# Kernel tuning notes

Measured on AMD Instinct MI355X. Metric: run time of the kernel, lower is better.

The kernel has to match this reference:

```python
import jax, jax.numpy as jnp
import numpy as np

DIM = 512

def setup_inputs() -> dict:
    key = jax.random.key(0)
    ks = jax.random.split(key, 7)
    B, Nq, Nkv = 8, 1024, 4096
    prototype = jax.random.normal(ks[0], (B, Nq, DIM), dtype=jnp.float32)
    q_x = jax.random.normal(ks[1], (B, Nkv, DIM), dtype=jnp.float32)
    qry_attn_mask = jax.random.bernoulli(ks[2], 0.5, (B, Nkv))  # True = keep
    # Linear(dim, dim, bias=False) weights, torch convention y = x @ W.T
    s = 1.0 / np.sqrt(DIM)
    Wq = jax.random.uniform(ks[3], (DIM, DIM), jnp.float32, -s, s)
    Wk = jax.random.uniform(ks[4], (DIM, DIM), jnp.float32, -s, s)
    Wv = jax.random.uniform(ks[5], (DIM, DIM), jnp.float32, -s, s)
    Wproj = jax.random.uniform(ks[6], (DIM, DIM), jnp.float32, -s, s)
    return {"prototype": prototype, "q_x": q_x, "qry_attn_mask": qry_attn_mask,
            "Wq": Wq, "Wk": Wk, "Wv": Wv, "Wproj": Wproj}

def reference(prototype, q_x, qry_attn_mask, Wq, Wk, Wv, Wproj):
    scale = DIM ** (-0.5)
    q = jnp.einsum('bnd,ed->bne', prototype, Wq)          # [B,Nq,D]
    k = jnp.einsum('bmd,ed->bme', q_x, Wk)                # [B,Nkv,D]
    v = jnp.einsum('bmd,ed->bme', q_x, Wv)                # [B,Nkv,D]
    attn = jnp.einsum('bnd,bmd->bnm', q, k) * scale       # [B,Nq,Nkv]
    bias = (~qry_attn_mask).astype(attn.dtype)[:, None, :] * -10000.0
    attn = jax.nn.softmax(attn + bias, axis=-1)
    x = jnp.einsum('bnm,bmd->bnd', attn, v)
    x = jnp.einsum('bnd,ed->bne', x, Wproj)
    return x
```

## Files before the change

### kernel.cpp

```cpp
#include <hip/hip_runtime.h>
#include <hip/hip_bf16.h>
#include <stdint.h>


typedef __bf16 bf16;
typedef bf16 bf16x8 __attribute__((ext_vector_type(8)));
typedef bf16 bf16x4 __attribute__((ext_vector_type(4)));
typedef float f32x4 __attribute__((ext_vector_type(4)));

#define NB 8
#define NQ 1024
#define NKV 4096
#define DD 512
#define RT_LD 136

__device__ __forceinline__ void lds16(const bf16* g, bf16* l) {
  __builtin_amdgcn_global_load_lds(
      (const __attribute__((address_space(1))) unsigned int*)g,
      (__attribute__((address_space(3))) unsigned int*)l, 16, 0, 0);
}

__global__ void scan_mask(const void* __restrict__ mask,
                          int* __restrict__ idx, int* __restrict__ cnt,
                          int* __restrict__ kpad, float* __restrict__ denom) {
  const int b = blockIdx.x, tid = threadIdx.x;
  for (int i = tid; i < NQ; i += 256) denom[b * NQ + i] = 0.f;

  __shared__ int s0, s1;
  if (tid == 0) { s0 = 0; s1 = 0; }
  __syncthreads();
  {
    const unsigned* mw = (const unsigned*)mask;
    int b0 = 0, b1 = 0;
    for (int i = tid; i < 8192; i += 256) {
      unsigned v = mw[i];
      if (v > 1u) b0 = 1;
      if (v != 0u && v != 0x3F800000u) b1 = 1;
    }
    if (b0) atomicOr(&s0, 1);
    if (b1) atomicOr(&s1, 1);
  }
  __syncthreads();
  const int mode = (s0 == 0) ? 0 : ((s1 == 0) ? 1 : 2);

  __shared__ int ps[256];
  unsigned bits = 0;
  int c = 0;
  const int base = tid * 16;
  for (int i = 0; i < 16; ++i) {
    const int col = base + i;
    bool k;
    if (mode == 0)      k = ((const int*)mask)[b * NKV + col] != 0;
    else if (mode == 1) k = ((const float*)mask)[b * NKV + col] != 0.f;
    else                k = ((const unsigned char*)mask)[b * NKV + col] != 0;
    bits |= (unsigned)k << i;
    c += k;
  }
  ps[tid] = c;
  __syncthreads();
  for (int s = 1; s < 256; s <<= 1) {
    int v = (tid >= s) ? ps[tid - s] : 0;
    __syncthreads();
    ps[tid] += v;
    __syncthreads();
  }
  int off = ps[tid] - c;
  for (int i = 0; i < 16; ++i)
    if ((bits >> i) & 1) idx[b * NKV + off++] = base + i;
  if (tid == 255) {
    cnt[b] = ps[255];
    kpad[b] = (ps[255] + 127) & ~127;
  }
}

__global__ void prep(const float* __restrict__ qx, const int* __restrict__ idx,
                     const int* __restrict__ cnt, const int* __restrict__ kpad,
                     bf16* __restrict__ qc,
                     const float* __restrict__ proto, bf16* __restrict__ proto_b,
                     const float* __restrict__ Wq, const float* __restrict__ Wk,
                     const float* __restrict__ Wv, const float* __restrict__ Wp,
                     bf16* __restrict__ Wq_b, bf16* __restrict__ Wkv_b,
                     bf16* __restrict__ Wp_b) {
  const int blk = blockIdx.x, tid = threadIdx.x;
  if (blk < 2048) {
    const int b = blk >> 8, bx = blk & 255;
    const int wave = tid >> 6, lane = tid & 63;
    const int r0 = bx * 16 + wave * 4;
    const int n = cnt[b];
    const int kp = kpad[b];
#pragma unroll
    for (int j = 0; j < 4; ++j) {
      const int row = r0 + j;
      if (row >= kp) return;
      bf16x4* d = (bf16x4*)(qc + ((long)b * NKV + row) * DD) + lane;
      if (row < n) {
        const int src = idx[b * NKV + row];
        const float4* s = (const float4*)(qx + ((long)b * NKV + src) * DD) + lane;
        float4 v0 = s[0], v1 = s[64];
        bf16x4 o0, o1;
        o0.x = (bf16)v0.x; o0.y = (bf16)v0.y; o0.z = (bf16)v0.z; o0.w = (bf16)v0.w;
        o1.x = (bf16)v1.x; o1.y = (bf16)v1.y; o1.z = (bf16)v1.z; o1.w = (bf16)v1.w;
        d[0] = o0;
        d[64] = o1;
      } else {
        bf16x4 z;
        z.x = (bf16)0.f; z.y = (bf16)0.f; z.z = (bf16)0.f; z.w = (bf16)0.f;
        d[0] = z;
        d[64] = z;
      }
    }
  } else if (blk < 6144) {
    const int i = (blk - 2048) * 256 + tid;
    float4 v = ((const float4*)proto)[i];
    bf16x4 o;
    o.x = (bf16)v.x; o.y = (bf16)v.y; o.z = (bf16)v.z; o.w = (bf16)v.w;
    ((bf16x4*)proto_b)[i] = o;
  } else {
    const int j = (blk - 6144) * 256 + tid;
    const int w = j >> 16, r = j & 65535;
    const float* src = (w == 0) ? Wq : (w == 1) ? Wk : (w == 2) ? Wv : Wp;
    bf16x4* dst = (w == 0) ? (bf16x4*)Wq_b
                : (w == 3) ? (bf16x4*)Wp_b
                           : (bf16x4*)Wkv_b + (w == 2 ? 65536 : 0);
    float4 v = ((const float4*)src)[r];
    bf16x4 o;
    o.x = (bf16)v.x; o.y = (bf16)v.y; o.z = (bf16)v.z; o.w = (bf16)v.w;
    dst[r] = o;
  }
}

template <int EPI>
__global__ void __launch_bounds__(256, 3)
gemm_bt(const bf16* __restrict__ A, const bf16* __restrict__ Bw,
        void* __restrict__ Cp, void* __restrict__ Cp2,
        int N, int Klen, int Kstride,
        long sA, long sB, long sC,
        const int* __restrict__ cnt, const int* __restrict__ kpad,
        float* __restrict__ denom, float scale, int M) {
  __shared__ alignas(16) bf16 Smem[24576];
  bf16* Rt = Smem;
  const int tid = threadIdx.x;
  const int wave = tid >> 6, lane = tid & 63;
  const int l15 = lane & 15, l4 = lane >> 4;
  const int wm = (wave >> 1) * 64, wn = (wave & 1) * 64;
  const int bx = (EPI == 5) ? blockIdx.y : blockIdx.x;
  const int by = (EPI == 5) ? blockIdx.x : blockIdx.y;
  const int b = blockIdx.z;

  if constexpr (EPI == 2) {
    if (bx * 128 >= kpad[b]) return;
  } else if constexpr (EPI == 5) {
    const int bb = by >> 5, loc = (by & 31) * 128;
    if (loc >= kpad[bb]) return;
  }

  const bf16* Ab = A + (long)b * sA + (long)(by * 128) * Kstride;
  const bf16* Bb = Bw + (long)b * sB + (long)(bx * 128) * Kstride;

  const int srow = lane >> 2, scol = (lane & 3) * 8;
  const int c0 = wave * 2, c1 = wave * 2 + 1;
  const bf16* g0 = Ab + (long)(c0 * 16 + srow) * Kstride + scol;
  const bf16* g1 = Ab + (long)(c1 * 16 + srow) * Kstride + scol;
  const bf16* g2 = Bb + (long)(c0 * 16 + srow) * Kstride + scol;
  const bf16* g3 = Bb + (long)(c1 * 16 + srow) * Kstride + scol;
  bf16* l0 = Smem + c0 * 512;
  bf16* l1 = Smem + c1 * 512;
  bf16* l2 = Smem + 4096 + c0 * 512;
  bf16* l3 = Smem + 4096 + c1 * 512;

  f32x4 acc[4][4] = {};
  const int nt = Klen >> 5;

#define GSTAGE(bb)                                            \
  do {                                                        \
    const int o_ = (bb) * 8192;                               \
    lds16(g0, l0 + o_); lds16(g1, l1 + o_);                   \
    lds16(g2, l2 + o_); lds16(g3, l3 + o_);                   \
    g0 += 32; g1 += 32; g2 += 32; g3 += 32;                   \
  } while (0)

  GSTAGE(0);
  GSTAGE(1);
  int rd = 0, wr = 2;
  for (int t = 0; t < nt; ++t) {
    if (t + 1 < nt) {
      asm volatile("s_waitcnt vmcnt(4)" ::: "memory");
    } else {
      asm volatile("s_waitcnt vmcnt(0)" ::: "memory");
    }
    __builtin_amdgcn_s_barrier();
    __builtin_amdgcn_sched_barrier(0);
    if (t + 2 < nt) GSTAGE(wr);
    wr = (wr == 2) ? 0 : wr + 1;
    const bf16* Ac = Smem + rd * 8192;
    const bf16* Bc = Ac + 4096;
    rd = (rd == 2) ? 0 : rd + 1;
    bf16x8 af[4], bfr[4];
#pragma unroll
    for (int t2 = 0; t2 < 4; ++t2) {
      af[t2]  = *(const bf16x8*)(Ac + (wm + t2 * 16 + l15) * 32 + l4 * 8);
      bfr[t2] = *(const bf16x8*)(Bc + (wn + t2 * 16 + l15) * 32 + l4 * 8);
    }
#pragma unroll
    for (int mt = 0; mt < 4; ++mt)
#pragma unroll
      for (int nt2 = 0; nt2 < 4; ++nt2)
        acc[mt][nt2] = __builtin_amdgcn_mfma_f32_16x16x32_bf16(af[mt], bfr[nt2],
                                                               acc[mt][nt2], 0, 0, 0);
  }
#undef GSTAGE
  __syncthreads();

  const int rowBase = by * 128 + wm;
  const int colBase = bx * 128 + wn;
  const int tR = by * 128;
  const int tC = bx * 128;

  if constexpr (EPI == 2) {
    bf16* C = (bf16*)Cp + (long)b * sC;
    const int nkeep = cnt[b];
    float rs[4][4];
#pragma unroll
    for (int mt = 0; mt < 4; ++mt)
#pragma unroll
      for (int r = 0; r < 4; ++r) rs[mt][r] = 0.f;
#pragma unroll
    for (int nt2 = 0; nt2 < 4; ++nt2) {
      const bool keep = (colBase + nt2 * 16 + l15) < nkeep;
#pragma unroll
      for (int mt = 0; mt < 4; ++mt)
#pragma unroll
        for (int r = 0; r < 4; ++r) {
          float p = keep ? __expf(acc[mt][nt2][r] * scale) : 0.f;
          rs[mt][r] += p;
          Rt[(wm + mt * 16 + l4 * 4 + r) * RT_LD + wn + nt2 * 16 + l15] = (bf16)p;
        }
    }
#pragma unroll
    for (int mt = 0; mt < 4; ++mt)
#pragma unroll
      for (int r = 0; r < 4; ++r) {
        float v = rs[mt][r];
        v += __shfl_xor(v, 1, 64);
        v += __shfl_xor(v, 2, 64);
        v += __shfl_xor(v, 4, 64);
        v += __shfl_xor(v, 8, 64);
        if (l15 == 0)
          atomicAdd(&denom[b * M + rowBase + mt * 16 + l4 * 4 + r], v);
      }
    __syncthreads();
    const int r0 = tid >> 2, cq = (tid & 3) * 32;
#pragma unroll
    for (int h = 0; h < 128; h += 64)
#pragma unroll
      for (int j = 0; j < 4; ++j) {
        bf16x8 v = *(const bf16x8*)(Rt + (r0 + h) * RT_LD + cq + j * 8);
        *(bf16x8*)(C + (long)(tR + r0 + h) * N + tC + cq + j * 8) = v;
      }
  } else if constexpr (EPI == 0) {
    bf16* C = (bf16*)Cp;
#pragma unroll
    for (int mt = 0; mt < 4; ++mt)
#pragma unroll
      for (int nt2 = 0; nt2 < 4; ++nt2)
#pragma unroll
        for (int r = 0; r < 4; ++r)
          Rt[(wm + mt * 16 + l4 * 4 + r) * RT_LD + wn + nt2 * 16 + l15] =
              (bf16)acc[mt][nt2][r];
    __syncthreads();
    const int r0 = tid >> 2, cq = (tid & 3) * 32;
#pragma unroll
    for (int h = 0; h < 128; h += 64)
#pragma unroll
      for (int j = 0; j < 4; ++j) {
        bf16x8 v = *(const bf16x8*)(Rt + (r0 + h) * RT_LD + cq + j * 8);
        *(bf16x8*)(C + (long)(tR + r0 + h) * N + tC + cq + j * 8) = v;
      }
  } else if constexpr (EPI == 4) {
    float* C = (float*)Cp;
#pragma unroll
    for (int mt = 0; mt < 4; ++mt)
#pragma unroll
      for (int nt2 = 0; nt2 < 4; ++nt2)
#pragma unroll
        for (int r = 0; r < 4; ++r)
          C[(long)(tR + wm + mt * 16 + l4 * 4 + r) * N + tC + wn + nt2 * 16 + l15] =
              acc[mt][nt2][r];
  } else {
    if (tC < 512) {
      bf16* C = (bf16*)Cp;
#pragma unroll
      for (int mt = 0; mt < 4; ++mt)
#pragma unroll
        for (int nt2 = 0; nt2 < 4; ++nt2)
#pragma unroll
          for (int r = 0; r < 4; ++r)
            Rt[(wm + mt * 16 + l4 * 4 + r) * RT_LD + wn + nt2 * 16 + l15] =
                (bf16)acc[mt][nt2][r];
      __syncthreads();
      const int r0 = tid >> 2, cq = (tid & 3) * 32;
#pragma unroll
      for (int h = 0; h < 128; h += 64)
#pragma unroll
        for (int j = 0; j < 4; ++j) {
          bf16x8 v = *(const bf16x8*)(Rt + (r0 + h) * RT_LD + cq + j * 8);
          *(bf16x8*)(C + (long)(tR + r0 + h) * 512 + tC + cq + j * 8) = v;
        }
    } else {
      bf16* C = (bf16*)Cp2;
#pragma unroll
      for (int mt = 0; mt < 4; ++mt) {
        const int r0 = wm + mt * 16 + l4 * 4;
#pragma unroll
        for (int nt2 = 0; nt2 < 4; ++nt2) {
          const int cloc = wn + nt2 * 16 + l15;
          bf16x4 o;
          o.x = (bf16)acc[mt][nt2][0]; o.y = (bf16)acc[mt][nt2][1];
          o.z = (bf16)acc[mt][nt2][2]; o.w = (bf16)acc[mt][nt2][3];
          *(bf16x4*)(Rt + cloc * RT_LD + r0) = o;
        }
      }
      __syncthreads();
      const int bb = tR >> 12, kvloc = tR & 4095;
      const int d0 = tid >> 2, kvq = (tid & 3) * 32;
#pragma unroll
      for (int h = 0; h < 128; h += 64)
#pragma unroll
        for (int j = 0; j < 4; ++j) {
          bf16x8 v = *(const bf16x8*)(Rt + (d0 + h) * RT_LD + kvq + j * 8);
          *(bf16x8*)(C + (long)bb * DD * NKV + (long)(tC - 512 + d0 + h) * NKV +
                     kvloc + kvq + j * 8) = v;
        }
    }
  }
}

__global__ void __launch_bounds__(256, 4)
pv_direct(const bf16* __restrict__ P, const bf16* __restrict__ vT,
          const float* __restrict__ denom, const int* __restrict__ kpad,
          bf16* __restrict__ x) {
  __shared__ alignas(16) bf16 Smem[18432];
  bf16* Rt = Smem;
  const int tid = threadIdx.x;
  const int wave = tid >> 6, lane = tid & 63;
  const int l15 = lane & 15, l4 = lane >> 4;
  const int wm = (wave >> 1) * 32, wn = (wave & 1) * 64;
  const int qB = blockIdx.x * 64;
  const int dB = blockIdx.y * 128;
  const int b = blockIdx.z;
  const int Kb = kpad[b];

  const bf16* Ab = P + (long)b * NQ * NKV + (long)qB * NKV;
  const bf16* Bb = vT + (long)b * DD * NKV + (long)dB * NKV;

  const int srow = lane >> 2, scol = (lane & 3) * 8;
  const int c0 = wave * 2, c1 = wave * 2 + 1;
  const bf16* ga  = Ab + (long)(wave * 16 + srow) * NKV + scol;
  const bf16* gb0 = Bb + (long)(c0 * 16 + srow) * NKV + scol;
  const bf16* gb1 = Bb + (long)(c1 * 16 + srow) * NKV + scol;
  bf16* la  = Smem + wave * 512;
  bf16* lb0 = Smem + 2048 + c0 * 512;
  bf16* lb1 = Smem + 2048 + c1 * 512;

  f32x4 acc[2][4] = {};
  const int nt = Kb >> 5;

#define PSTAGE(bb)                                           \
  do {                                                       \
    const int o_ = (bb) * 6144;                              \
    lds16(ga, la + o_); lds16(gb0, lb0 + o_);                \
    lds16(gb1, lb1 + o_);                                    \
    ga += 32; gb0 += 32; gb1 += 32;                          \
  } while (0)

  PSTAGE(0);
  PSTAGE(1);
  int rd = 0, wr = 2;
  for (int t = 0; t < nt; ++t) {
    if (t + 1 < nt) {
      asm volatile("s_waitcnt vmcnt(3)" ::: "memory");
    } else {
      asm volatile("s_waitcnt vmcnt(0)" ::: "memory");
    }
    __builtin_amdgcn_s_barrier();
    __builtin_amdgcn_sched_barrier(0);
    if (t + 2 < nt) PSTAGE(wr);
    wr = (wr == 2) ? 0 : wr + 1;
    const bf16* Ac = Smem + rd * 6144;
    const bf16* Bc = Ac + 2048;
    rd = (rd == 2) ? 0 : rd + 1;
    bf16x8 af[2], bfr[4];
#pragma unroll
    for (int t2 = 0; t2 < 2; ++t2)
      af[t2] = *(const bf16x8*)(Ac + (wm + t2 * 16 + l15) * 32 + l4 * 8);
#pragma unroll
    for (int t2 = 0; t2 < 4; ++t2)
      bfr[t2] = *(const bf16x8*)(Bc + (wn + t2 * 16 + l15) * 32 + l4 * 8);
#pragma unroll
    for (int mt = 0; mt < 2; ++mt)
#pragma unroll
      for (int nt2 = 0; nt2 < 4; ++nt2)
        acc[mt][nt2] = __builtin_amdgcn_mfma_f32_16x16x32_bf16(af[mt], bfr[nt2],
                                                               acc[mt][nt2], 0, 0, 0);
  }
#undef PSTAGE
  __syncthreads();

#pragma unroll
  for (int mt = 0; mt < 2; ++mt)
#pragma unroll
    for (int r = 0; r < 4; ++r) {
      const int row = wm + mt * 16 + l4 * 4 + r;
      const float inv = 1.0f / denom[b * NQ + qB + row];
#pragma unroll
      for (int nt2 = 0; nt2 < 4; ++nt2)
        Rt[row * RT_LD + wn + nt2 * 16 + l15] = (bf16)(acc[mt][nt2][r] * inv);
    }
  __syncthreads();
  const int r0 = tid >> 2, cq = (tid & 3) * 32;
#pragma unroll
  for (int j = 0; j < 4; ++j) {
    bf16x8 v = *(const bf16x8*)(Rt + r0 * RT_LD + cq + j * 8);
    *(bf16x8*)(x + (long)(b * NQ + qB + r0) * DD + dB + cq + j * 8) = v;
  }
}

extern "C" void kernel_launch(void* const* d_in, const int* in_sizes, int n_in,
                              void* d_out, int out_size, void* d_ws, size_t ws_size,
                              hipStream_t stream) {
  const float* proto = (const float*)d_in[0];
  const float* qx    = (const float*)d_in[1];
  const void*  mask  = d_in[2];
  const float* Wq    = (const float*)d_in[3];
  const float* Wk    = (const float*)d_in[4];
  const float* Wv    = (const float*)d_in[5];
  const float* Wproj = (const float*)d_in[6];
  float* out = (float*)d_out;

  char* w = (char*)d_ws;
  int*   cnt   = (int*)(w + 64);
  int*   kpadA = (int*)(w + 128);
  float* denom = (float*)(w + 4096);
  size_t off = 65536;
  bf16* Wq_b  = (bf16*)(w + off); off += (size_t)DD * DD * 2;
  bf16* Wkv_b = (bf16*)(w + off); off += (size_t)DD * DD * 4;
  bf16* Wp_b  = (bf16*)(w + off); off += (size_t)DD * DD * 2;
  int*  idx   = (int*)(w + off);  off += (size_t)NB * NKV * 4;
  bf16* q_b   = (bf16*)(w + off); off += (size_t)NB * NQ * DD * 2;
  bf16* k_b   = (bf16*)(w + off); off += (size_t)NB * NKV * DD * 2;
  bf16* vT_b  = (bf16*)(w + off); off += (size_t)NB * NKV * DD * 2;
  bf16* x_b   = (bf16*)(w + off); off += (size_t)NB * NQ * DD * 2;
  size_t off_pp = off;
  bf16* proto_b = (bf16*)(w + off); off += (size_t)NB * NQ * DD * 2;
  bf16* qc_b    = (bf16*)(w + off);
  bf16* P       = (bf16*)(w + off_pp);

  scan_mask<<<8, 256, 0, stream>>>(mask, idx, cnt, kpadA, denom);
  prep<<<7168, 256, 0, stream>>>(qx, idx, cnt, kpadA, qc_b,
                                 proto, proto_b, Wq, Wk, Wv, Wproj,
                                 Wq_b, Wkv_b, Wp_b);

  const float scale = 0.04419417382415922f;

  gemm_bt<0><<<dim3(4, 64, 1), 256, 0, stream>>>(
      proto_b, Wq_b, q_b, nullptr, DD, DD, DD, 0L, 0L, 0L,
      cnt, kpadA, nullptr, 0.f, 0);
  gemm_bt<5><<<dim3(256, 8, 1), 256, 0, stream>>>(
      qc_b, Wkv_b, k_b, vT_b, 1024, DD, DD, 0L, 0L, 0L,
      cnt, kpadA, nullptr, 0.f, 0);
  gemm_bt<2><<<dim3(NKV / 128, NQ / 128, NB), 256, 0, stream>>>(
      q_b, k_b, P, nullptr, NKV, DD, DD,
      (long)NQ * DD, (long)NKV * DD, (long)NQ * NKV,
      cnt, kpadA, denom, scale, NQ);
  pv_direct<<<dim3(16, 4, 8), 256, 0, stream>>>(P, vT_b, denom, kpadA, x_b);
  gemm_bt<4><<<dim3(4, 64, 1), 256, 0, stream>>>(
      x_b, Wp_b, out, nullptr, DD, DD, DD, 0L, 0L, 0L,
      cnt, kpadA, nullptr, 0.f, 0);
}
```

Measured before the change: 308.3 us.

## Replace QK^T score GEMM with 256x256-tile 512-thread kernel

Adds a dedicated score GEMM kernel (sgemm256) that uses 256x256 output tiles with 8 waves, double-buffered K-chunks loaded straight into LDS, and raised scheduling priority around the MFMA loops. The fused exp/row-sum/atomic denominator epilogue is kept and writes through LDS in two halves. Larger tiles halve global reads of Q and K per output and cut the number of atomic adds, aiming to reduce the memory traffic of the biggest GEMM. In exchange it uses 128KB of LDS with one block per CU, fewer blocks overall, coarser skipping of masked key tiles at 256 granularity, and computes exp twice in the epilogue.

Result: no change. 310.4 us (+0.7%).

```diff
diff --git a/kernel.cpp b/kernel.cpp
--- a/kernel.cpp
+++ b/kernel.cpp
@@ -13,6 +13,7 @@
 #define NKV 4096
 #define DD 512
 #define RT_LD 136
+#define RT2_LD 264
 
 __device__ __forceinline__ void lds16(const bf16* g, bf16* l) {
   __builtin_amdgcn_global_load_lds(
@@ -129,6 +130,138 @@
   }
 }
 
+__global__ void __launch_bounds__(512, 1)
+sgemm256(const bf16* __restrict__ A, const bf16* __restrict__ Bw,
+         bf16* __restrict__ P, const int* __restrict__ cnt,
+         const int* __restrict__ kpad, float* __restrict__ denom, float scale) {
+  __shared__ alignas(16) bf16 Smem[65536];
+  const int tid = threadIdx.x;
+  const int wave = tid >> 6, lane = tid & 63;
+  const int l15 = lane & 15, l4 = lane >> 4;
+  const int wm = wave >> 2, wn = wave & 3;
+  const int bx = blockIdx.x, by = blockIdx.y, b = blockIdx.z;
+  if (bx * 256 >= kpad[b]) return;
+
+  const bf16* Ab = A + (long)b * NQ * DD + (long)(by * 256) * DD;
+  const bf16* Bb = Bw + (long)b * NKV * DD + (long)(bx * 256) * DD;
+  const int srow = lane >> 2, scol = (lane & 3) * 8;
+  const int s0 = wave, s1 = wave + 8;
+  const bf16* aG0 = Ab + (long)(s0 * 16 + srow) * DD + scol;
+  const bf16* aG1 = Ab + (long)(s1 * 16 + srow) * DD + scol;
+  const bf16* bG0 = Bb + (long)(s0 * 16 + srow) * DD + scol;
+  const bf16* bG1 = Bb + (long)(s1 * 16 + srow) * DD + scol;
+  bf16* aL0 = Smem + s0 * 512;
+  bf16* aL1 = Smem + s1 * 512;
+  bf16* bL0 = Smem + 16384 + s0 * 512;
+  bf16* bL1 = Smem + 16384 + s1 * 512;
+
+  f32x4 acc[8][4] = {};
+
+#pragma unroll
+  for (int kh = 0; kh < 2; ++kh) {
+    const int o = kh * 8192;
+    lds16(aG0 + kh * 32, aL0 + o);
+    lds16(aG1 + kh * 32, aL1 + o);
+    lds16(bG0 + kh * 32, bL0 + o);
+    lds16(bG1 + kh * 32, bL1 + o);
+  }
+
+  for (int t = 0; t < 8; ++t) {
+    const int d = (t & 1) * 32768;
+#pragma unroll
+    for (int kh = 0; kh < 2; ++kh) {
+      if (t < 7 || kh == 0)
+        asm volatile("s_waitcnt vmcnt(4)" ::: "memory");
+      else
+        asm volatile("s_waitcnt vmcnt(0)" ::: "memory");
+      __builtin_amdgcn_s_barrier();
+      __builtin_amdgcn_sched_barrier(0);
+      if (t < 7) {
+        const int dn = (d ^ 32768) + kh * 8192;
+        const long ko = (long)(t + 1) * 64 + kh * 32;
+        lds16(aG0 + ko, aL0 + dn);
+        lds16(aG1 + ko, aL1 + dn);
+        lds16(bG0 + ko, bL0 + dn);
+        lds16(bG1 + ko, bL1 + dn);
+      }
+      bf16x8 af[8], bfr[4];
+      const bf16* Ap = Smem + d + kh * 8192 + wm * 4096 + l15 * 32 + l4 * 8;
+      const bf16* Bp = Smem + d + 16384 + kh * 8192 + wn * 2048 + l15 * 32 + l4 * 8;
+#pragma unroll
+      for (int mt = 0; mt < 8; ++mt) af[mt] = *(const bf16x8*)(Ap + mt * 512);
+#pragma unroll
+      for (int nt = 0; nt < 4; ++nt) bfr[nt] = *(const bf16x8*)(Bp + nt * 512);
+      __builtin_amdgcn_s_setprio(1);
+#pragma unroll
+      for (int mt = 0; mt < 8; ++mt)
+#pragma unroll
+        for (int nt = 0; nt < 4; ++nt)
+          acc[mt][nt] = __builtin_amdgcn_mfma_f32_16x16x32_bf16(
+              af[mt], bfr[nt], acc[mt][nt], 0, 0, 0);
+      __builtin_amdgcn_s_setprio(0);
+    }
+  }
+  __syncthreads();
+
+  const int nkeep = cnt[b];
+  const int tR = by * 256, tC = bx * 256;
+  bf16* Cb = P + (long)b * NQ * NKV;
+
+  float rs[8][4];
+#pragma unroll
+  for (int mt = 0; mt < 8; ++mt)
+#pragma unroll
+    for (int r = 0; r < 4; ++r) rs[mt][r] = 0.f;
+#pragma unroll
+  for (int nt = 0; nt < 4; ++nt) {
+    const bool keep = (tC + wn * 64 + nt * 16 + l15) < nkeep;
+#pragma unroll
+    for (int mt = 0; mt < 8; ++mt)
+#pragma unroll
+      for (int r = 0; r < 4; ++r)
+        rs[mt][r] += keep ? __expf(acc[mt][nt][r] * scale) : 0.f;
+  }
+#pragma unroll
+  for (int mt = 0; mt < 8; ++mt)
+#pragma unroll
+    for (int r = 0; r < 4; ++r) {
+      float v = rs[mt][r];
+      v += __shfl_xor(v, 1, 64);
+      v += __shfl_xor(v, 2, 64);
+      v += __shfl_xor(v, 4, 64);
+      v += __shfl_xor(v, 8, 64);
+      if (l15 == 0)
+        atomicAdd(&denom[b * NQ + tR + wm * 128 + mt * 16 + l4 * 4 + r], v);
+    }
+
+  bf16* Rt = Smem;
+  const int r0 = tid >> 2, cb = (tid & 3) * 64;
+#pragma unroll
+  for (int h = 0; h < 2; ++h) {
+    if (wm == h) {
+#pragma unroll
+      for (int nt = 0; nt < 4; ++nt) {
+        const bool keep = (tC + wn * 64 + nt * 16 + l15) < nkeep;
+#pragma unroll
+        for (int mt = 0; mt < 8; ++mt)
+#pragma unroll
+          for (int r = 0; r < 4; ++r) {
+            float p = keep ? __expf(acc[mt][nt][r] * scale) : 0.f;
+            Rt[(mt * 16 + l4 * 4 + r) * RT2_LD + wn * 64 + nt * 16 + l15] =
+                (bf16)p;
+          }
+      }
+    }
+    __syncthreads();
+#pragma unroll
+    for (int j = 0; j < 8; ++j) {
+      bf16x8 v = *(const bf16x8*)(Rt + r0 * RT2_LD + cb + j * 8);
+      *(bf16x8*)(Cb + (long)(tR + h * 128 + r0) * NKV + tC + cb + j * 8) = v;
+    }
+    __syncthreads();
+  }
+}
+
 template <int EPI>
 __global__ void __launch_bounds__(256, 3)
 gemm_bt(const bf16* __restrict__ A, const bf16* __restrict__ Bw,
@@ -147,9 +280,7 @@
   const int by = (EPI == 5) ? blockIdx.x : blockIdx.y;
   const int b = blockIdx.z;
 
-  if constexpr (EPI == 2) {
-    if (bx * 128 >= kpad[b]) return;
-  } else if constexpr (EPI == 5) {
+  if constexpr (EPI == 5) {
     const int bb = by >> 5, loc = (by & 31) * 128;
     if (loc >= kpad[bb]) return;
   }
@@ -211,53 +342,10 @@
 #undef GSTAGE
   __syncthreads();
 
-  const int rowBase = by * 128 + wm;
-  const int colBase = bx * 128 + wn;
   const int tR = by * 128;
   const int tC = bx * 128;
 
-  if constexpr (EPI == 2) {
-    bf16* C = (bf16*)Cp + (long)b * sC;
-    const int nkeep = cnt[b];
-    float rs[4][4];
-#pragma unroll
-    for (int mt = 0; mt < 4; ++mt)
-#pragma unroll
-      for (int r = 0; r < 4; ++r) rs[mt][r] = 0.f;
-#pragma unroll
-    for (int nt2 = 0; nt2 < 4; ++nt2) {
-      const bool keep = (colBase + nt2 * 16 + l15) < nkeep;
-#pragma unroll
-      for (int mt = 0; mt < 4; ++mt)
-#pragma unroll
-        for (int r = 0; r < 4; ++r) {
-          float p = keep ? __expf(acc[mt][nt2][r] * scale) : 0.f;
-          rs[mt][r] += p;
-          Rt[(wm + mt * 16 + l4 * 4 + r) * RT_LD + wn + nt2 * 16 + l15] = (bf16)p;
-        }
-    }
-#pragma unroll
-    for (int mt = 0; mt < 4; ++mt)
-#pragma unroll
-      for (int r = 0; r < 4; ++r) {
-        float v = rs[mt][r];
-        v += __shfl_xor(v, 1, 64);
-        v += __shfl_xor(v, 2, 64);
-        v += __shfl_xor(v, 4, 64);
-        v += __shfl_xor(v, 8, 64);
-        if (l15 == 0)
-          atomicAdd(&denom[b * M + rowBase + mt * 16 + l4 * 4 + r], v);
-      }
-    __syncthreads();
-    const int r0 = tid >> 2, cq = (tid & 3) * 32;
-#pragma unroll
-    for (int h = 0; h < 128; h += 64)
-#pragma unroll
-      for (int j = 0; j < 4; ++j) {
-        bf16x8 v = *(const bf16x8*)(Rt + (r0 + h) * RT_LD + cq + j * 8);
-        *(bf16x8*)(C + (long)(tR + r0 + h) * N + tC + cq + j * 8) = v;
-      }
-  } else if constexpr (EPI == 0) {
+  if constexpr (EPI == 0) {
     bf16* C = (bf16*)Cp;
 #pragma unroll
     for (int mt = 0; mt < 4; ++mt)
@@ -468,10 +556,8 @@
   gemm_bt<5><<<dim3(256, 8, 1), 256, 0, stream>>>(
       qc_b, Wkv_b, k_b, vT_b, 1024, DD, DD, 0L, 0L, 0L,
       cnt, kpadA, nullptr, 0.f, 0);
-  gemm_bt<2><<<dim3(NKV / 128, NQ / 128, NB), 256, 0, stream>>>(
-      q_b, k_b, P, nullptr, NKV, DD, DD,
-      (long)NQ * DD, (long)NKV * DD, (long)NQ * NKV,
-      cnt, kpadA, denom, scale, NQ);
+  sgemm256<<<dim3(NKV / 256, NQ / 256, NB), 512, 0, stream>>>(
+      q_b, k_b, P, cnt, kpadA, denom, scale);
   pv_direct<<<dim3(16, 4, 8), 256, 0, stream>>>(P, vT_b, denom, kpadA, x_b);
   gemm_bt<4><<<dim3(4, 64, 1), 256, 0, stream>>>(
       x_b, Wp_b, out, nullptr, DD, DD, DD, 0L, 0L, 0L,
```
